# Performance work log

Hardware: AMD Instinct MI355X
Metric: run time of the kernel (lower is better)

## Reference

```python
import jax, jax.numpy as jnp
import numpy as np

N = 100000   # nodes per node type ('net' and 'cell')
E = 600000   # edges per canonical relation
D_IN = 16    # raw input feature dim
D = 128      # hidden dim (in_size == out_size, required by wl: Linear(2*D -> D))
SLOPE = 0.2  # DGL GATConv leaky_relu negative slope


def setup_inputs() -> dict:
    key = jax.random.key(0)
    ks = jax.random.split(key, 24)
    f = lambda k, shp, scale=1.0: jax.random.normal(k, shp, dtype=jnp.float32) * scale
    s_in = 1.0 / np.sqrt(D_IN).astype(np.float32)
    s_d = 1.0 / np.sqrt(D).astype(np.float32)
    s_2d = 1.0 / np.sqrt(2 * D).astype(np.float32)
    inp = {
        'x_net':   f(ks[0], (N, D_IN)),
        'x_cell':  f(ks[1], (N, D_IN)),
        'Wp_net':  f(ks[2], (D, D_IN), s_in),
        'Wp_cell': f(ks[3], (D, D_IN), s_in),
        # per-edge-type GATConv params: fc weight + attn_l + attn_r (num_heads=1, no bias)
        'Wg0': f(ks[4], (D, D), s_d), 'al0': f(ks[5], (D,), s_d), 'ar0': f(ks[6], (D,), s_d),
        'Wg1': f(ks[7], (D, D), s_d), 'al1': f(ks[8], (D,), s_d), 'ar1': f(ks[9], (D,), s_d),
        'Wg2': f(ks[10], (D, D), s_d), 'al2': f(ks[11], (D,), s_d), 'ar2': f(ks[12], (D,), s_d),
        'Wl':   f(ks[13], (D, 2 * D), s_2d),
        'bias': jnp.zeros((D,), jnp.float32),
        # edge lists: relation 0 = cell->net, 1 = net->cell, 2 = net->net
        'src0': jax.random.randint(ks[14], (E,), 0, N, dtype=jnp.int32),
        'dst0': jax.random.randint(ks[15], (E,), 0, N, dtype=jnp.int32),
        'src1': jax.random.randint(ks[16], (E,), 0, N, dtype=jnp.int32),
        'dst1': jax.random.randint(ks[17], (E,), 0, N, dtype=jnp.int32),
        'src2': jax.random.randint(ks[18], (E,), 0, N, dtype=jnp.int32),
        'dst2': jax.random.randint(ks[19], (E,), 0, N, dtype=jnp.int32),
    }
    return inp


def _gat(x_src, x_dst, W, al, ar, src, dst):
    """DGL GATConv (num_heads=1, bias=False) on one relation's edge list."""
    h_src = x_src @ W.T                               # [N, D]
    h_dst = x_dst @ W.T                               # [N, D]
    el = (h_src @ al)[src]                            # [E] gathered src logits
    er = (h_dst @ ar)[dst]                            # [E] gathered dst logits
    e = jax.nn.leaky_relu(el + er, SLOPE)             # [E]
    # segment softmax over incoming edges of each dst node
    m = jax.ops.segment_max(e, dst, num_segments=N)
    ex = jnp.exp(e - m[dst])
    denom = jax.ops.segment_sum(ex, dst, num_segments=N)
    alpha = ex / denom[dst]                           # [E]
    return jax.ops.segment_sum(h_src[src] * alpha[:, None], dst, num_segments=N)


def reference(x_net, x_cell, Wp_net, Wp_cell,
              Wg0, al0, ar0, Wg1, al1, ar1, Wg2, al2, ar2,
              Wl, bias,
              src0, dst0, src1, dst1, src2, dst2):
    # feature projection per node type (ParaGraph.feat_proj)
    h_net = x_net @ Wp_net.T                          # [N, D]
    h_cell = x_cell @ Wp_cell.T                       # [N, D]
    feat = {'net': h_net, 'cell': h_cell}
    out = {'net': jnp.zeros((N, D), h_net.dtype), 'cell': jnp.zeros((N, D), h_cell.dtype)}
    # canonical etypes: (srctype, dsttype, gat params, edge list)
    rels = [
        ('cell', 'net', Wg0, al0, ar0, src0, dst0),
        ('net', 'cell', Wg1, al1, ar1, src1, dst1),
        ('net', 'net',  Wg2, al2, ar2, src2, dst2),
    ]
    for st, dt, W, al, ar, src, dst in rels:
        out[dt] = out[dt] + _gat(feat[st], feat[dt], W, al, ar, src, dst)
        # faithful to the original: concat+linear+relu recomputed for EVERY ntype
        # inside the etype loop (the redundant fused-op pattern)
        for nt in ('net', 'cell'):
            out[nt] = jax.nn.relu(
                jnp.concatenate([feat[nt], out[nt] + bias], axis=1) @ Wl.T)
    return jnp.stack([out['net'], out['cell']])      # [2, N, D]
```

## Files before the change

### kernel.cpp

```cpp
#include <hip/hip_runtime.h>
#include <hip/hip_bf16.h>
#include <stdint.h>

#define NN 100000
#define NE 600000
#define SP 136
#define NB 782
#define BCAP 1600
#define CHUNK 4096
#define NCH 147
#define GB 1563
#define AB 6250

typedef unsigned short u16;
typedef unsigned int u32;
typedef __attribute__((ext_vector_type(8))) short short8;
typedef __attribute__((ext_vector_type(8))) __bf16 bf16x8;
typedef __attribute__((ext_vector_type(4))) float floatx4;

__device__ __forceinline__ float b2f(u16 u) {
  union { float f; u32 i; } c; c.i = ((u32)u) << 16; return c.f;
}
__device__ __forceinline__ u16 f2b(float f) {
  union { float f; u32 i; } c; c.f = f;
  u32 r = c.i + 0x7FFFu + ((c.i >> 16) & 1u);
  return (u16)(r >> 16);
}


__device__ __forceinline__ void gemm_w(const u16* __restrict__ W, int ldw, u16* __restrict__ C,
                                       u16* lds, int tid, int row0, const bf16x8* a,
                                       int m16, int quad, int wv) {
#pragma unroll
  for (int it = 0; it < 8; ++it) {
    int idx = it * 256 + tid;
    int r = idx >> 4, c = (idx & 15) << 3;
    *(short8*)(&lds[r * SP + c]) = *(const short8*)(W + (size_t)r * ldw + c);
  }
  __syncthreads();
  const u16* brow = &lds[m16 * SP + quad * 8];
  floatx4 acc[8];
#pragma unroll
  for (int c = 0; c < 8; ++c) acc[c] = floatx4{0.f, 0.f, 0.f, 0.f};
#pragma unroll
  for (int kk = 0; kk < 4; ++kk) {
#pragma unroll
    for (int c = 0; c < 8; ++c) {
      bf16x8 bfr = *(const bf16x8*)(brow + c * 16 * SP + kk * 32);
      acc[c] = __builtin_amdgcn_mfma_f32_16x16x32_bf16(a[kk], bfr, acc[c], 0, 0, 0);
    }
  }
#pragma unroll
  for (int c = 0; c < 8; ++c) {
    int col = c * 16 + m16;
#pragma unroll
    for (int r = 0; r < 4; ++r) {
      int grow = row0 + wv * 16 + quad * 4 + r;
      if (grow < NN) C[(size_t)grow * 128 + col] = f2b(acc[c][r]);
    }
  }
}

__device__ __forceinline__ void stageW2(const u16* __restrict__ W2, u16* Wlds, int tid) {
#pragma unroll
  for (int it = 0; it < 8; ++it) {
    int idx = it * 256 + tid;
    int r = idx >> 4, c = (idx & 15) << 3;
    *(short8*)(&Wlds[r * SP + c]) = *(const short8*)(W2 + (size_t)r * 256 + c);
  }
}

template<int INIT>
__device__ __forceinline__ void gat_phase(int nb, int tid, const u16* __restrict__ h,
                                          const u32* __restrict__ srecs,
                                          const float* __restrict__ walpha,
                                          const int* __restrict__ rp, u16* Alds) {
  int sub = tid & 15, g = tid >> 4;
  int n = nb * 16 + g;
  int start = rp[n], end = rp[n + 1];
  float row[8];
  if (INIT) {
    short8 pv = *(const short8*)(&Alds[g * SP + sub * 8]);
#pragma unroll
    for (int t = 0; t < 8; ++t) row[t] = b2f((u16)pv[t]);
  } else {
#pragma unroll
    for (int t = 0; t < 8; ++t) row[t] = 0.f;
  }
  if (start < end) {
    float acc[8];
#pragma unroll
    for (int t = 0; t < 8; ++t) acc[t] = 0.f;
    const u16* hsub = h + sub * 8;
    int e = start;
    for (; e + 4 <= end; e += 4) {
      int s0 = (int)srecs[e],     s1 = (int)srecs[e + 1];
      int s2 = (int)srecs[e + 2], s3 = (int)srecs[e + 3];
      float x0 = walpha[e],     x1 = walpha[e + 1];
      float x2 = walpha[e + 2], x3 = walpha[e + 3];
      short8 h0 = *(const short8*)(hsub + (size_t)s0 * 128);
      short8 h1 = *(const short8*)(hsub + (size_t)s1 * 128);
      short8 h2 = *(const short8*)(hsub + (size_t)s2 * 128);
      short8 h3 = *(const short8*)(hsub + (size_t)s3 * 128);
#pragma unroll
      for (int t = 0; t < 8; ++t) {
        acc[t] += x0 * b2f((u16)h0[t]) + x1 * b2f((u16)h1[t])
                + x2 * b2f((u16)h2[t]) + x3 * b2f((u16)h3[t]);
      }
    }
    for (; e < end; ++e) {
      int sv = (int)srecs[e];
      float x = walpha[e];
      short8 hv = *(const short8*)(hsub + (size_t)sv * 128);
#pragma unroll
      for (int t = 0; t < 8; ++t) acc[t] += x * b2f((u16)hv[t]);
    }
#pragma unroll
    for (int t = 0; t < 8; ++t) row[t] += acc[t];
  }
  short8 rb;
#pragma unroll
  for (int t = 0; t < 8; ++t) rb[t] = (short)f2b(row[t]);
  *(short8*)(&Alds[g * SP + sub * 8]) = rb;
}

template<int TO_GLOBAL>
__device__ __forceinline__ void F_phase(int nb, int tid, const u16* __restrict__ P,
                                        const float* __restrict__ cvec,
                                        const u16* Wlds, u16* Alds, void* __restrict__ out) {
  const int lane = tid & 63, wv = tid >> 6;
  const int m16 = lane & 15, quad = lane >> 4;
  const u16* arow = &Alds[m16 * SP + quad * 8];
  bf16x8 a[4];
#pragma unroll
  for (int kk = 0; kk < 4; ++kk) a[kk] = *(const bf16x8*)(arow + kk * 32);
  if (!TO_GLOBAL) __syncthreads();
  const u16* brow = &Wlds[m16 * SP + quad * 8];
  floatx4 acc2[2];
#pragma unroll
  for (int cc = 0; cc < 2; ++cc) acc2[cc] = floatx4{0.f, 0.f, 0.f, 0.f};
#pragma unroll
  for (int kk = 0; kk < 4; ++kk) {
#pragma unroll
    for (int cc = 0; cc < 2; ++cc) {
      int ct = wv * 2 + cc;
      bf16x8 bfr = *(const bf16x8*)(brow + ct * 16 * SP + kk * 32);
      acc2[cc] = __builtin_amdgcn_mfma_f32_16x16x32_bf16(a[kk], bfr, acc2[cc], 0, 0, 0);
    }
  }
#pragma unroll
  for (int cc = 0; cc < 2; ++cc) {
    int ct = wv * 2 + cc;
    int col = ct * 16 + m16;
    float cv = cvec[col];
#pragma unroll
    for (int r = 0; r < 4; ++r) {
      int nrow = quad * 4 + r;
      int node = nb * 16 + nrow;
      float v = acc2[cc][r] + b2f(P[(size_t)node * 128 + col]) + cv;
      v = fmaxf(v, 0.f);
      if (TO_GLOBAL) ((float*)out)[(size_t)node * 128 + col] = v;
      else           Alds[nrow * SP + col] = f2b(v);
    }
  }
  if (!TO_GLOBAL) __syncthreads();
}


__global__ __launch_bounds__(256) void prep_k(const float* __restrict__ x_net, const float* __restrict__ x_cell,
                                              const float* __restrict__ Wp_net, const float* __restrict__ Wp_cell,
                                              u16* __restrict__ feat_net, u16* __restrict__ feat_cell,
                                              const float* __restrict__ Wl, const float* __restrict__ Wg0,
                                              const float* __restrict__ Wg1, const float* __restrict__ Wg2,
                                              u16* __restrict__ Wl_bf, u16* __restrict__ Wg_bf,
                                              const float* al0, const float* ar0, const float* al1,
                                              const float* ar1, const float* al2, const float* ar2,
                                              const float* bias, float* __restrict__ vecs,
                                              int* __restrict__ bcnt) {
  int bid = blockIdx.x, tid = threadIdx.x;
  if (bid < 2 * AB) {
    int y = bid >= AB;
    int bx = y ? bid - AB : bid;
    const float* x  = y ? x_cell : x_net;
    const float* Wp = y ? Wp_cell : Wp_net;
    u16* feat       = y ? feat_cell : feat_net;
    __shared__ float Ws[128 * 17];
    __shared__ float xs[16][17];
#pragma unroll
    for (int it = 0; it < 8; ++it) {
      int idx = it * 256 + tid;
      int j = idx >> 4, k = idx & 15;
      Ws[j * 17 + k] = Wp[idx];
    }
    int n0 = bx * 16;
    { int nn = tid >> 4, k = tid & 15;
      xs[nn][k] = x[(size_t)(n0 + nn) * 16 + k]; }
    __syncthreads();
    int j = tid & 127, g = tid >> 7;
    float acc[8];
#pragma unroll
    for (int r = 0; r < 8; ++r) acc[r] = 0.f;
#pragma unroll
    for (int k = 0; k < 16; ++k) {
      float w = Ws[j * 17 + k];
#pragma unroll
      for (int r = 0; r < 8; ++r) acc[r] += xs[g * 8 + r][k] * w;
    }
#pragma unroll
    for (int r = 0; r < 8; ++r)
      feat[(size_t)(n0 + g * 8 + r) * 128 + j] = f2b(acc[r]);
  } else if (bid < 2 * AB + 128) {
    int cid = bid - 2 * AB;
    int y = cid >> 5, bx = cid & 31;
    const float* src = (y == 0) ? Wl : (y == 1) ? Wg0 : (y == 2) ? Wg1 : Wg2;
    u16* dst = (y == 0) ? Wl_bf : Wg_bf + (size_t)(y - 1) * 16384;
    int n = (y == 0) ? 32768 : 16384;
    int i = (bx * 256 + tid) * 4;
    if (i >= n) return;
    float4 v = *(const float4*)(src + i);
    ushort4 p; p.x = f2b(v.x); p.y = f2b(v.y); p.z = f2b(v.z); p.w = f2b(v.w);
    *(ushort4*)(dst + i) = p;
  } else if (bid < 2 * AB + 135) {
    int a = bid - (2 * AB + 128);
    if (tid >= 128) return;
    int j = tid;
    float s = 0.f;
    if (a < 6) {
      const float* W = (a < 2) ? Wg0 : (a < 4) ? Wg1 : Wg2;
      const float* v = (a == 0) ? al0 : (a == 1) ? ar0 : (a == 2) ? al1 : (a == 3) ? ar1 : (a == 4) ? al2 : ar2;
      for (int i = 0; i < 128; ++i) s += W[i * 128 + j] * v[i];
    } else {
      for (int i = 0; i < 128; ++i) s += Wl[(size_t)j * 256 + 128 + i] * bias[i];
    }
    vecs[a * 128 + j] = s;
  } else {
    int r = bid - (2 * AB + 135);
    for (int i = tid; i < NB; i += 256) bcnt[(size_t)r * NB + i] = 0;
  }
}

__global__ __launch_bounds__(256) void logbh_k(const u16* __restrict__ feat_net, const u16* __restrict__ feat_cell,
                                               const float* __restrict__ vecs, float* __restrict__ outs,
                                               const int* __restrict__ dst0, const int* __restrict__ dst1,
                                               const int* __restrict__ dst2, int* __restrict__ bcnt) {
  __shared__ int sm[NB];
  int bid = blockIdx.x, tid = threadIdx.x;
  if (bid < 782) {
    float* vs = (float*)sm;
#pragma unroll
    for (int it = 0; it < 3; ++it) vs[it * 256 + tid] = vecs[it * 256 + tid];
    __syncthreads();
    int y = bid >= 391;
    int bx = y ? bid - 391 : bid;
    const u16* f = y ? feat_cell : feat_net;
    int n = bx * 256 + tid;
    if (n >= NN) return;
    const u16* row = f + (size_t)n * 128;
    if (y == 0) {
      float s1 = 0.f, s2 = 0.f, s4 = 0.f, s5 = 0.f;
#pragma unroll
      for (int k = 0; k < 128; k += 8) {
        short8 u = *(const short8*)(row + k);
#pragma unroll
        for (int t = 0; t < 8; ++t) {
          float fv = b2f((u16)u[t]);
          s1 += fv * vs[1 * 128 + k + t]; s2 += fv * vs[2 * 128 + k + t];
          s4 += fv * vs[4 * 128 + k + t]; s5 += fv * vs[5 * 128 + k + t];
        }
      }
      outs[(size_t)1 * NN + n] = s1; outs[(size_t)2 * NN + n] = s2;
      outs[(size_t)4 * NN + n] = s4; outs[(size_t)5 * NN + n] = s5;
    } else {
      float s0 = 0.f, s3 = 0.f;
#pragma unroll
      for (int k = 0; k < 128; k += 8) {
        short8 u = *(const short8*)(row + k);
#pragma unroll
        for (int t = 0; t < 8; ++t) {
          float fv = b2f((u16)u[t]);
          s0 += fv * vs[0 * 128 + k + t]; s3 += fv * vs[3 * 128 + k + t];
        }
      }
      outs[(size_t)0 * NN + n] = s0; outs[(size_t)3 * NN + n] = s3;
    }
  } else {
    int e = bid - 782;
    int r = e / NCH, bx = e % NCH;
    const int* dst = (r == 0) ? dst0 : (r == 1) ? dst1 : dst2;
    for (int i = tid; i < NB; i += 256) sm[i] = 0;
    __syncthreads();
    int e0 = bx * CHUNK;
    int cnt = NE - e0; if (cnt > CHUNK) cnt = CHUNK;
    for (int i = tid; i < cnt; i += 256) atomicAdd(&sm[((u32)dst[e0 + i]) >> 7], 1);
    __syncthreads();
    for (int b = tid; b < NB; b += 256) {
      int c = sm[b];
      if (c) atomicAdd(&bcnt[(size_t)r * NB + b], c);
    }
  }
}

__global__ __launch_bounds__(1024) void bscan_k(const int* __restrict__ bcnt, int* __restrict__ bptr,
                                                int* __restrict__ bcur) {
  int r = blockIdx.x, t = threadIdx.x;
  const int* c = bcnt + (size_t)r * NB;
  int* p = bptr + (size_t)r * (NB + 1);
  int* cur = bcur + (size_t)r * NB;
  int v = (t < NB) ? c[t] : 0;
  __shared__ int ss[1024];
  ss[t] = v; __syncthreads();
  for (int off = 1; off < 1024; off <<= 1) {
    int u = (t >= off) ? ss[t - off] : 0;
    __syncthreads();
    ss[t] += u;
    __syncthreads();
  }
  if (t < NB) { int e = ss[t] - v; p[t] = e; cur[t] = e; }
  if (t == 1023) p[NB] = ss[1023];
}

__global__ __launch_bounds__(256) void bscatter_k(const int* __restrict__ src0, const int* __restrict__ dst0,
                                                  const int* __restrict__ src1, const int* __restrict__ dst1,
                                                  const int* __restrict__ src2, const int* __restrict__ dst2,
                                                  int* __restrict__ bcur, u32* __restrict__ recs) {
  int r = blockIdx.y;
  const int* src = (r == 0) ? src0 : (r == 1) ? src1 : src2;
  const int* dst = (r == 0) ? dst0 : (r == 1) ? dst1 : dst2;
  __shared__ int hist[NB];
  __shared__ int lstart[NB];
  __shared__ int lcur[NB];
  __shared__ int badj[NB];
  __shared__ u32 rbuf[CHUNK];
  __shared__ u16 kbuf[CHUNK];
  __shared__ int ss[256];
  int tid = threadIdx.x;
  int e0 = blockIdx.x * CHUNK;
  int cnt = NE - e0; if (cnt > CHUNK) cnt = CHUNK;

  for (int i = tid; i < NB; i += 256) hist[i] = 0;
  __syncthreads();
  for (int i = tid; i < cnt; i += 256) atomicAdd(&hist[((u32)dst[e0 + i]) >> 7], 1);
  __syncthreads();
  int loc[4]; int s = 0;
  int base4 = tid * 4;
#pragma unroll
  for (int j = 0; j < 4; ++j) {
    int idx = base4 + j;
    int v = (idx < NB) ? hist[idx] : 0;
    loc[j] = s; s += v;
  }
  ss[tid] = s; __syncthreads();
  for (int off = 1; off < 256; off <<= 1) {
    int u = (tid >= off) ? ss[tid - off] : 0;
    __syncthreads();
    ss[tid] += u;
    __syncthreads();
  }
  int ex = ss[tid] - s;
#pragma unroll
  for (int j = 0; j < 4; ++j) {
    int idx = base4 + j;
    if (idx < NB) { int e = ex + loc[j]; lstart[idx] = e; lcur[idx] = e; }
  }
  __syncthreads();
  for (int b = tid; b < NB; b += 256) {
    int c = hist[b];
    int g = 0;
    if (c) g = atomicAdd(&bcur[(size_t)r * NB + b], c);
    badj[b] = g - lstart[b];
  }
  __syncthreads();
  for (int i = tid; i < cnt; i += 256) {
    int dN = dst[e0 + i], sN = src[e0 + i];
    int b = ((u32)dN) >> 7;
    int pos = atomicAdd(&lcur[b], 1);
    rbuf[pos] = ((u32)(dN & 127) << 17) | (u32)sN;
    kbuf[pos] = (u16)b;
  }
  __syncthreads();
  u32* out = recs + (size_t)r * NE;
  for (int i = tid; i < cnt; i += 256) {
    int b = kbuf[i];
    out[badj[b] + i] = rbuf[i];
  }
}

__global__ __launch_bounds__(256) void sortgemm_k(u32* __restrict__ recs, const int* __restrict__ bptr,
                                                  int* __restrict__ rowptr,
                                                  const u16* __restrict__ feat_net, const u16* __restrict__ feat_cell,
                                                  const u16* __restrict__ Wl_bf, const u16* __restrict__ Wg_bf,
                                                  u16* __restrict__ P_net, u16* __restrict__ P_cell,
                                                  u16* __restrict__ h0, u16* __restrict__ h1, u16* __restrict__ h2,
                                                  const float* __restrict__ logit, float* __restrict__ walpha) {
  __shared__ u32 smem[128 * SP / 2];
  int bid = blockIdx.x, tid = threadIdx.x;
  if (bid < 2 * GB) {
    int ntype = bid >= GB;
    int blk = ntype ? bid - GB : bid;
    u16* lds = (u16*)smem;
    const u16* A = ntype ? feat_cell : feat_net;
    const int row0 = blk * 64;
    const int lane = tid & 63, wv = tid >> 6;
    const int m16 = lane & 15, quad = lane >> 4;
    int arow = row0 + wv * 16 + m16;
    if (arow >= NN) arow = NN - 1;
    const u16* Ab = A + (size_t)arow * 128 + quad * 8;
    bf16x8 a[4];
#pragma unroll
    for (int kk = 0; kk < 4; ++kk) a[kk] = *(const bf16x8*)(Ab + kk * 32);
    if (!ntype) {
      gemm_w(Wl_bf,          256, P_net, lds, tid, row0, a, m16, quad, wv);
      __syncthreads();
      gemm_w(Wg_bf + 16384,  128, h1,    lds, tid, row0, a, m16, quad, wv);
      __syncthreads();
      gemm_w(Wg_bf + 32768,  128, h2,    lds, tid, row0, a, m16, quad, wv);
    } else {
      gemm_w(Wl_bf,          256, P_cell, lds, tid, row0, a, m16, quad, wv);
      __syncthreads();
      gemm_w(Wg_bf,          128, h0,     lds, tid, row0, a, m16, quad, wv);
    }
  } else {
    int sb = bid - 2 * GB;
    int r = sb / NB, b = sb % NB;
    const int* p = bptr + (size_t)r * (NB + 1);
    u32* rec = recs + (size_t)r * NE;
    float* wal = walpha + (size_t)r * NE;
    int* rp = rowptr + (size_t)r * (NN + 1);
    const float* el = logit + (size_t)(2 * r) * NN;
    const float* er = logit + (size_t)(2 * r + 1) * NN;
    int base = p[b], end = p[b + 1];
    int cnt = end - base; if (cnt > BCAP) cnt = BCAP;
    u32* rs = smem;
    float* xs = (float*)(smem + BCAP);
    int* hist = (int*)(smem + 2 * BCAP);
    int* excl = hist + 128;
    int* cur  = excl + 128;
    float* den = (float*)(cur + 128);
    float* ers = den + 128;
    for (int i = tid; i < cnt; i += 256) rs[i] = rec[base + i];
    if (tid < 128) {
      hist[tid] = 0;
      den[tid] = 0.f;
      int node = b * 128 + tid;
      ers[tid] = (node < NN) ? er[node] : 0.f;
    }
    __syncthreads();
    for (int i = tid; i < cnt; i += 256) {
      u32 v = rs[i];
      int d = v >> 17;
      float l = el[v & 0x1FFFFu] + ers[d];
      l = (l >= 0.f) ? l : 0.2f * l;
      float x = __expf(l);
      xs[i] = x;
      atomicAdd(&den[d], x);
      atomicAdd(&hist[d], 1);
    }
    __syncthreads();
    if (tid < 128) cur[tid] = hist[tid];
    __syncthreads();
    for (int off = 1; off < 128; off <<= 1) {
      int v = 0;
      if (tid < 128 && tid >= off) v = cur[tid - off];
      __syncthreads();
      if (tid < 128) cur[tid] += v;
      __syncthreads();
    }
    if (tid < 128) {
      int e = cur[tid] - hist[tid];
      excl[tid] = e;
      int node = b * 128 + tid;
      if (node < NN) rp[node] = base + e;
      float dd = den[tid];
      den[tid] = (dd > 0.f) ? 1.f / dd : 0.f;
    }
    if (b == NB - 1 && tid == 0) rp[NN] = p[NB];
    if (tid < 128) cur[tid] = excl[tid];
    __syncthreads();
    for (int i = tid; i < cnt; i += 256) {
      u32 v = rs[i];
      int d = v >> 17;
      int pos = atomicAdd(&cur[d], 1);
      rec[base + pos] = v & 0x1FFFFu;
      wal[base + pos] = xs[i] * den[d];
    }
  }
}

__global__ __launch_bounds__(256) void tail_k(const u16* __restrict__ h0, const u16* __restrict__ h1,
                                              const u16* __restrict__ h2,
                                              const u32* __restrict__ recs, const float* __restrict__ walpha,
                                              const int* __restrict__ rowptr,
                                              const u16* __restrict__ P_net, const u16* __restrict__ P_cell,
                                              const u16* __restrict__ W2, const float* __restrict__ cvec,
                                              float* __restrict__ out_net, float* __restrict__ out_cell) {
  __shared__ u16 Wlds[128 * SP];
  __shared__ u16 Alds[16 * SP];
  int bid = blockIdx.x, tid = threadIdx.x;
  stageW2(W2, Wlds, tid);
  if (bid < AB) {
    int nb = bid;
    gat_phase<0>(nb, tid, h0, recs, walpha, rowptr, Alds);
    __syncthreads();
    F_phase<0>(nb, tid, P_net, cvec, Wlds, Alds, nullptr);
    F_phase<0>(nb, tid, P_net, cvec, Wlds, Alds, nullptr);
    gat_phase<1>(nb, tid, h2, recs + (size_t)2 * NE, walpha + (size_t)2 * NE,
                 rowptr + 2 * (NN + 1), Alds);
    __syncthreads();
    F_phase<1>(nb, tid, P_net, cvec, Wlds, Alds, (void*)out_net);
  } else {
    int nb = bid - AB;
    {
      int sub = tid & 15, g = tid >> 4;
      int n = nb * 16 + g;
      short8 pv = *(const short8*)(P_cell + (size_t)n * 128 + sub * 8);
      short8 rb;
#pragma unroll
      for (int t = 0; t < 8; ++t)
        rb[t] = (short)f2b(fmaxf(b2f((u16)pv[t]) + cvec[sub * 8 + t], 0.f));
      *(short8*)(&Alds[g * SP + sub * 8]) = rb;
    }
    gat_phase<1>(nb, tid, h1, recs + (size_t)NE, walpha + (size_t)NE,
                 rowptr + (NN + 1), Alds);
    __syncthreads();
    F_phase<0>(nb, tid, P_cell, cvec, Wlds, Alds, nullptr);
    F_phase<1>(nb, tid, P_cell, cvec, Wlds, Alds, (void*)out_cell);
  }
}

extern "C" void kernel_launch(void* const* d_in, const int* in_sizes, int n_in,
                              void* d_out, int out_size, void* d_ws, size_t ws_size,
                              hipStream_t stream) {
  const float* x_net   = (const float*)d_in[0];
  const float* x_cell  = (const float*)d_in[1];
  const float* Wp_net  = (const float*)d_in[2];
  const float* Wp_cell = (const float*)d_in[3];
  const float* Wg[3] = {(const float*)d_in[4], (const float*)d_in[7], (const float*)d_in[10]};
  const float* al[3] = {(const float*)d_in[5], (const float*)d_in[8], (const float*)d_in[11]};
  const float* ar[3] = {(const float*)d_in[6], (const float*)d_in[9], (const float*)d_in[12]};
  const float* Wl    = (const float*)d_in[13];
  const float* bias  = (const float*)d_in[14];
  const int* src[3] = {(const int*)d_in[15], (const int*)d_in[17], (const int*)d_in[19]};
  const int* dst[3] = {(const int*)d_in[16], (const int*)d_in[18], (const int*)d_in[20]};

  char* ws = (char*)d_ws;
  size_t off = 0;
  auto alloc = [&](size_t b) { void* p = ws + off; off = (off + b + 255) & ~(size_t)255; return p; };
  u16*  feat_net  = (u16*)alloc((size_t)NN * 128 * 2);
  u16*  feat_cell = (u16*)alloc((size_t)NN * 128 * 2);
  u16*  hbuf0     = (u16*)alloc((size_t)NN * 128 * 2);
  u16*  hbuf1     = (u16*)alloc((size_t)NN * 128 * 2);
  u16*  hbuf2     = (u16*)alloc((size_t)NN * 128 * 2);
  u16*  P_net     = (u16*)alloc((size_t)NN * 128 * 2);
  u16*  P_cell    = (u16*)alloc((size_t)NN * 128 * 2);
  float* vecs     = (float*)alloc(7 * 128 * 4);
  float* logit    = (float*)alloc((size_t)6 * NN * 4);
  u16*   Wl_bf    = (u16*)alloc((size_t)128 * 256 * 2);
  u16*   Wg_bf    = (u16*)alloc((size_t)3 * 128 * 128 * 2);
  int*   bcnt     = (int*)alloc((size_t)3 * NB * 4);
  int*   bcur     = (int*)alloc((size_t)3 * NB * 4);
  int*   bptr     = (int*)alloc((size_t)3 * (NB + 1) * 4);
  int*   rowptr   = (int*)alloc((size_t)3 * (NN + 1) * 4);
  u32*   recs     = (u32*)alloc((size_t)3 * NE * 4);
  float* walpha   = (float*)alloc((size_t)3 * NE * 4);

  float* out_f = (float*)d_out;
  const u16* W2 = Wl_bf + 128;
  const float* cvec = vecs + 6 * 128;

  prep_k<<<2 * AB + 138, 256, 0, stream>>>(x_net, x_cell, Wp_net, Wp_cell, feat_net, feat_cell,
                                           Wl, Wg[0], Wg[1], Wg[2], Wl_bf, Wg_bf,
                                           al[0], ar[0], al[1], ar[1], al[2], ar[2], bias, vecs, bcnt);
  logbh_k<<<782 + 3 * NCH, 256, 0, stream>>>(feat_net, feat_cell, vecs, logit,
                                             dst[0], dst[1], dst[2], bcnt);
  bscan_k<<<3, 1024, 0, stream>>>(bcnt, bptr, bcur);
  bscatter_k<<<dim3(NCH, 3), 256, 0, stream>>>(src[0], dst[0], src[1], dst[1], src[2], dst[2],
                                               bcur, recs);
  sortgemm_k<<<2 * GB + 3 * NB, 256, 0, stream>>>(recs, bptr, rowptr, feat_net, feat_cell,
                                                  Wl_bf, Wg_bf, P_net, P_cell, hbuf0, hbuf1, hbuf2,
                                                  logit, walpha);
  tail_k<<<2 * AB, 256, 0, stream>>>(hbuf0, hbuf1, hbuf2, recs, walpha, rowptr,
                                     P_net, P_cell, W2, cvec,
                                     out_f, out_f + (size_t)NN * 128);
}
```

Baseline: 423.4 us.

## Interleave both net-relation GAT gathers in one pass before the F phases

```diff
diff --git a/kernel.cpp b/kernel.cpp
--- a/kernel.cpp
+++ b/kernel.cpp
@@ -93,27 +93,25 @@
     for (int t = 0; t < 8; ++t) acc[t] = 0.f;
     const u16* hsub = h + sub * 8;
     int e = start;
-    for (; e + 4 <= end; e += 4) {
-      int s0 = (int)srecs[e],     s1 = (int)srecs[e + 1];
-      int s2 = (int)srecs[e + 2], s3 = (int)srecs[e + 3];
-      float x0 = walpha[e],     x1 = walpha[e + 1];
-      float x2 = walpha[e + 2], x3 = walpha[e + 3];
-      short8 h0 = *(const short8*)(hsub + (size_t)s0 * 128);
-      short8 h1 = *(const short8*)(hsub + (size_t)s1 * 128);
-      short8 h2 = *(const short8*)(hsub + (size_t)s2 * 128);
-      short8 h3 = *(const short8*)(hsub + (size_t)s3 * 128);
-#pragma unroll
-      for (int t = 0; t < 8; ++t) {
-        acc[t] += x0 * b2f((u16)h0[t]) + x1 * b2f((u16)h1[t])
-                + x2 * b2f((u16)h2[t]) + x3 * b2f((u16)h3[t]);
+    for (; e < end; e += 4) {
+      int m = end - e; if (m > 4) m = 4;
+      int s[4]; float x[4]; short8 hv[4];
+#pragma unroll
+      for (int j = 0; j < 4; ++j) {
+        if (j < m) { s[j] = (int)srecs[e + j]; x[j] = walpha[e + j]; }
       }
-    }
-    for (; e < end; ++e) {
-      int sv = (int)srecs[e];
-      float x = walpha[e];
-      short8 hv = *(const short8*)(hsub + (size_t)sv * 128);
-#pragma unroll
-      for (int t = 0; t < 8; ++t) acc[t] += x * b2f((u16)hv[t]);
+#pragma unroll
+      for (int j = 0; j < 4; ++j) {
+        if (j < m) hv[j] = *(const short8*)(hsub + (size_t)s[j] * 128);
+      }
+#pragma unroll
+      for (int j = 0; j < 4; ++j) {
+        if (j < m) {
+          float xx = x[j];
+#pragma unroll
+          for (int t = 0; t < 8; ++t) acc[t] += xx * b2f((u16)hv[j][t]);
+        }
+      }
     }
 #pragma unroll
     for (int t = 0; t < 8; ++t) row[t] += acc[t];
@@ -122,6 +120,60 @@
 #pragma unroll
   for (int t = 0; t < 8; ++t) rb[t] = (short)f2b(row[t]);
   *(short8*)(&Alds[g * SP + sub * 8]) = rb;
+}
+
+__device__ __forceinline__ void gat_dual(int n, int sub,
+                                         const u16* __restrict__ hA, const u32* __restrict__ srA,
+                                         const float* __restrict__ waA, const int* __restrict__ rpA,
+                                         const u16* __restrict__ hB, const u32* __restrict__ srB,
+                                         const float* __restrict__ waB, const int* __restrict__ rpB,
+                                         float* accA, float* accB) {
+  int eA = rpA[n], endA = rpA[n + 1];
+  int eB = rpB[n], endB = rpB[n + 1];
+#pragma unroll
+  for (int t = 0; t < 8; ++t) { accA[t] = 0.f; accB[t] = 0.f; }
+  const u16* hsubA = hA + sub * 8;
+  const u16* hsubB = hB + sub * 8;
+  while (eA < endA || eB < endB) {
+    int mA = endA - eA; if (mA > 4) mA = 4;
+    int mB = endB - eB; if (mB > 4) mB = 4;
+    int sA[4], sB[4]; float xA[4], xB[4];
+#pragma unroll
+    for (int j = 0; j < 4; ++j) {
+      if (j < mA) { sA[j] = (int)srA[eA + j]; xA[j] = waA[eA + j]; }
+    }
+#pragma unroll
+    for (int j = 0; j < 4; ++j) {
+      if (j < mB) { sB[j] = (int)srB[eB + j]; xB[j] = waB[eB + j]; }
+    }
+    short8 hvA[4], hvB[4];
+#pragma unroll
+    for (int j = 0; j < 4; ++j) {
+      if (j < mA) hvA[j] = *(const short8*)(hsubA + (size_t)sA[j] * 128);
+    }
+#pragma unroll
+    for (int j = 0; j < 4; ++j) {
+      if (j < mB) hvB[j] = *(const short8*)(hsubB + (size_t)sB[j] * 128);
+    }
+#pragma unroll
+    for (int j = 0; j < 4; ++j) {
+      if (j < mA) {
+        float x = xA[j];
+#pragma unroll
+        for (int t = 0; t < 8; ++t) accA[t] += x * b2f((u16)hvA[j][t]);
+      }
+    }
+#pragma unroll
+    for (int j = 0; j < 4; ++j) {
+      if (j < mB) {
+        float x = xB[j];
+#pragma unroll
+        for (int t = 0; t < 8; ++t) accB[t] += x * b2f((u16)hvB[j][t]);
+      }
+    }
+    if (mA > 0) eA += mA;
+    if (mB > 0) eB += mB;
+  }
 }
 
 template<int TO_GLOBAL>
@@ -497,20 +549,33 @@
   __shared__ u16 Alds[16 * SP];
   int bid = blockIdx.x, tid = threadIdx.x;
   stageW2(W2, Wlds, tid);
+  int sub = tid & 15, g = tid >> 4;
   if (bid < AB) {
     int nb = bid;
-    gat_phase<0>(nb, tid, h0, recs, walpha, rowptr, Alds);
+    int n = nb * 16 + g;
+    float accA[8], accB[8];
+    gat_dual(n, sub, h0, recs, walpha, rowptr,
+             h2, recs + (size_t)2 * NE, walpha + (size_t)2 * NE, rowptr + 2 * (NN + 1),
+             accA, accB);
+    short8 rb;
+#pragma unroll
+    for (int t = 0; t < 8; ++t) rb[t] = (short)f2b(accA[t]);
+    *(short8*)(&Alds[g * SP + sub * 8]) = rb;
     __syncthreads();
     F_phase<0>(nb, tid, P_net, cvec, Wlds, Alds, nullptr);
     F_phase<0>(nb, tid, P_net, cvec, Wlds, Alds, nullptr);
-    gat_phase<1>(nb, tid, h2, recs + (size_t)2 * NE, walpha + (size_t)2 * NE,
-                 rowptr + 2 * (NN + 1), Alds);
+    {
+      short8 pv = *(const short8*)(&Alds[g * SP + sub * 8]);
+      short8 nv;
+#pragma unroll
+      for (int t = 0; t < 8; ++t) nv[t] = (short)f2b(b2f((u16)pv[t]) + accB[t]);
+      *(short8*)(&Alds[g * SP + sub * 8]) = nv;
+    }
     __syncthreads();
     F_phase<1>(nb, tid, P_net, cvec, Wlds, Alds, (void*)out_net);
   } else {
     int nb = bid - AB;
     {
-      int sub = tid & 15, g = tid >> 4;
       int n = nb * 16 + g;
       short8 pv = *(const short8*)(P_cell + (size_t)n * 128 + sub * 8);
       short8 rb;
```

New measurement: 461.1 us. +8.9%, slower.
